# Performance work log

Hardware: AMD Instinct MI355X
Metric: run time of the kernel (lower is better)

The kernel has to match this reference:

```python
import jax, jax.numpy as jnp
import numpy as np

EMBED_DIM = 1024
NUM_HEADS = 16
HEAD_DIM = EMBED_DIM // NUM_HEADS
BOARD = 32
SEQ = BOARD * BOARD
BATCH = 16


def setup_inputs() -> dict:
    key = jax.random.key(0)
    ks = jax.random.split(key, 6)
    x = jax.random.normal(ks[0], (BATCH, SEQ, EMBED_DIM), dtype=jnp.float32)
    scale = 1.0 / np.sqrt(EMBED_DIM)
    Wq = jax.random.normal(ks[1], (EMBED_DIM, EMBED_DIM), dtype=jnp.float32) * scale
    Wk = jax.random.normal(ks[2], (EMBED_DIM, EMBED_DIM), dtype=jnp.float32) * scale
    Wv = jax.random.normal(ks[3], (EMBED_DIM, EMBED_DIM), dtype=jnp.float32) * scale
    Wo = jax.random.normal(ks[4], (EMBED_DIM, EMBED_DIM), dtype=jnp.float32) * scale
    rel_bias = jax.random.normal(ks[5], (NUM_HEADS, 2 * BOARD - 1), dtype=jnp.float32)
    return {"x": x, "Wq": Wq, "Wk": Wk, "Wv": Wv, "Wo": Wo, "rel_bias": rel_bias}


def _rel_indices():
    # coords of the flattened H*W grid
    idx = jnp.arange(SEQ)
    rows = idx // BOARD
    cols = idx % BOARD
    offset = BOARD - 1
    rel_x = cols[None, :] - cols[:, None] + offset  # [S, S]
    rel_y = rows[None, :] - rows[:, None] + offset  # [S, S]
    return rel_x, rel_y


def reference(x, Wq, Wk, Wv, Wo, rel_bias):
    B, S, E = x.shape
    H, D = NUM_HEADS, HEAD_DIM
    # projections (Linear with bias=False: x @ W.T; weights here stored as [E, E] applied as x @ W)
    q = (x @ Wq).reshape(B, S, H, D).transpose(0, 2, 1, 3)  # [B,H,S,D]
    k = (x @ Wk).reshape(B, S, H, D).transpose(0, 2, 1, 3)
    v = (x @ Wv).reshape(B, S, H, D).transpose(0, 2, 1, 3)
    scores = jnp.einsum('bhqd,bhkd->bhqk', q, k) / jnp.sqrt(jnp.float32(D))
    rel_x, rel_y = _rel_indices()
    bias = rel_bias[:, rel_x] + rel_bias[:, rel_y]  # [H, S, S]
    scores = scores + bias[None]
    attn = jax.nn.softmax(scores, axis=-1)
    out = jnp.einsum('bhqk,bhkd->bhqd', attn, v)
    out = out.transpose(0, 2, 1, 3).reshape(B, S, E)
    return out @ Wo
```

## Files before the change

kernel.cpp:

```cpp
#include <hip/hip_runtime.h>

#define SEQ   1024
#define EMBED 1024
#define NH    16
#define HD    64
#define NB    16

typedef float facc4 __attribute__((ext_vector_type(4)));
typedef float facc16 __attribute__((ext_vector_type(16)));
typedef short frag8 __attribute__((ext_vector_type(8)));
typedef short sv4 __attribute__((ext_vector_type(4)));

__device__ __forceinline__ unsigned short f2bf(float f) {
  union { float f; unsigned int u; } c; c.f = f;
  unsigned int u = c.u;
  u += 0x7FFFu + ((u >> 16) & 1u);
  return (unsigned short)(u >> 16);
}

__device__ __forceinline__ unsigned int pk_bf16(float lo, float hi) {
  unsigned int r;
  asm("v_cvt_pk_bf16_f32 %0, %1, %2" : "=v"(r) : "v"(lo), "v"(hi));
  return r;
}

__device__ __forceinline__ void gl_lds16(const void* g, void* l) {
  __builtin_amdgcn_global_load_lds(
      (const __attribute__((address_space(1))) unsigned int*)g,
      (__attribute__((address_space(3))) unsigned int*)l, 16, 0, 0);
}

__global__ __launch_bounds__(256) void convert_x_kernel(
    const float* __restrict__ x, unsigned short* __restrict__ xb, int n8) {
  int stride = gridDim.x * blockDim.x;
  for (int i = blockIdx.x * blockDim.x + threadIdx.x; i < n8; i += stride) {
    const float4* src = (const float4*)(x + (size_t)i * 8);
    float4 v0 = src[0], v1 = src[1];
    frag8 o;
    o[0] = f2bf(v0.x); o[1] = f2bf(v0.y); o[2] = f2bf(v0.z); o[3] = f2bf(v0.w);
    o[4] = f2bf(v1.x); o[5] = f2bf(v1.y); o[6] = f2bf(v1.z); o[7] = f2bf(v1.w);
    *(frag8*)(xb + (size_t)i * 8) = o;
  }
}

__global__ __launch_bounds__(256) void transpose_w_kernel(
    const float* W0, const float* W1, const float* W2, const float* W3,
    unsigned short* T0, unsigned short* T1, unsigned short* T2, unsigned short* T3) {
  __shared__ float tw[64][65];
  const float* W; unsigned short* T;
  switch (blockIdx.z) {
    case 0: W = W0; T = T0; break;
    case 1: W = W1; T = T1; break;
    case 2: W = W2; T = T2; break;
    default: W = W3; T = T3; break;
  }
  int k0 = blockIdx.y * 64, n0 = blockIdx.x * 64;
  int t = threadIdx.x;
#pragma unroll
  for (int rep = 0; rep < 4; ++rep) {
    int c = rep * 256 + t;
    int row = c >> 4, ch = c & 15;
    float4 v = *(const float4*)(W + (size_t)(k0 + row) * 1024 + n0 + ch * 4);
    tw[row][ch * 4 + 0] = v.x; tw[row][ch * 4 + 1] = v.y;
    tw[row][ch * 4 + 2] = v.z; tw[row][ch * 4 + 3] = v.w;
  }
  __syncthreads();
#pragma unroll
  for (int rep = 0; rep < 2; ++rep) {
    int c = rep * 256 + t;
    int nrow = c >> 3, ch = c & 7;
    frag8 o;
#pragma unroll
    for (int i = 0; i < 8; ++i) o[i] = (short)f2bf(tw[ch * 8 + i][nrow]);
    *(frag8*)(T + (size_t)(n0 + nrow) * 1024 + k0 + ch * 8) = o;
  }
}

template <int MODE>
__global__ __launch_bounds__(512, 2) void gemm256(
    const unsigned short* __restrict__ A, const unsigned short* __restrict__ Bt,
    unsigned short* __restrict__ qo, unsigned short* __restrict__ ko,
    unsigned short* __restrict__ vto, float* __restrict__ fo, int N) {
  __shared__ unsigned short a_s[2][256 * 64];
  __shared__ unsigned short b_s[2][256 * 64];
  const int tid = threadIdx.x;
  const int w = tid >> 6, l = tid & 63;
  const int l31 = l & 31, hi = l >> 5;
  const int wr = w >> 2, wc = w & 3;

  const int bid = blockIdx.x;
  const int xcd = bid & 7, j = bid >> 3;
  const int mt = xcd * 8 + (j & 7), nt = j >> 3;
  const int m0 = mt << 8, n0 = nt << 8;

  const int ldrow = l >> 3;
  const int swz8 = ((l & 7) ^ (ldrow & 7)) << 3;
  const unsigned short* Ab = A + (size_t)m0 * 1024;
  const unsigned short* Bb = Bt + (size_t)n0 * 1024;

  facc16 acc[4][2];
#pragma unroll
  for (int mi = 0; mi < 4; ++mi)
#pragma unroll
    for (int nj = 0; nj < 2; ++nj)
#pragma unroll
      for (int r = 0; r < 16; ++r) acc[mi][nj][r] = 0.f;

  auto STAGE = [&](int buf, int kt) {
#pragma unroll
    for (int i = 0; i < 4; ++i) {
      const int c = (w << 2) + i;
      gl_lds16(Ab + (size_t)kt * 64 + (size_t)((c << 3) + ldrow) * 1024 + swz8,
               &a_s[buf][c << 9]);
      gl_lds16(Bb + (size_t)kt * 64 + (size_t)((c << 3) + ldrow) * 1024 + swz8,
               &b_s[buf][c << 9]);
    }
  };

  STAGE(0, 0);
  STAGE(1, 1);
  asm volatile("s_waitcnt vmcnt(8)" ::: "memory");
  __builtin_amdgcn_s_barrier();
  __builtin_amdgcn_sched_barrier(0);

  const int rowA = (wr << 7) + l31;
  const int rowB = (wc << 6) + l31;
  const int swl = l31 & 7;

  for (int t = 0; t < 16; ++t) {
    const int cur = t & 1;
    const char* ap = (const char*)a_s[cur];
    const char* bp = (const char*)b_s[cur];
    frag8 af[4][2], bfv[2][2];

#pragma unroll
    for (int js2 = 0; js2 < 2; ++js2) {
      const int pc = (((js2 << 1) + hi) ^ swl) << 4;
#pragma unroll
      for (int mi = 0; mi < 4; ++mi)
        af[mi][js2] = *(const frag8*)(ap + (rowA + (mi << 5)) * 128 + pc);
#pragma unroll
      for (int nj = 0; nj < 2; ++nj)
        bfv[nj][js2] = *(const frag8*)(bp + (rowB + (nj << 5)) * 128 + pc);
    }
    __builtin_amdgcn_s_setprio(1);
#pragma unroll
    for (int js2 = 0; js2 < 2; ++js2)
#pragma unroll
      for (int mi = 0; mi < 4; ++mi)
#pragma unroll
        for (int nj = 0; nj < 2; ++nj)
          acc[mi][nj] = __builtin_amdgcn_mfma_f32_32x32x16_bf16(
              af[mi][js2], bfv[nj][js2], acc[mi][nj], 0, 0, 0);
    __builtin_amdgcn_s_setprio(0);

#pragma unroll
    for (int js2 = 0; js2 < 2; ++js2) {
      const int pc = ((((js2 + 2) << 1) + hi) ^ swl) << 4;
#pragma unroll
      for (int mi = 0; mi < 4; ++mi)
        af[mi][js2] = *(const frag8*)(ap + (rowA + (mi << 5)) * 128 + pc);
#pragma unroll
      for (int nj = 0; nj < 2; ++nj)
        bfv[nj][js2] = *(const frag8*)(bp + (rowB + (nj << 5)) * 128 + pc);
    }
    asm volatile("s_waitcnt lgkmcnt(0)" ::: "memory");
    __builtin_amdgcn_s_barrier();
    __builtin_amdgcn_sched_barrier(0);
    if (t + 2 < 16) STAGE(cur, t + 2);

    __builtin_amdgcn_s_setprio(1);
#pragma unroll
    for (int js2 = 0; js2 < 2; ++js2)
#pragma unroll
      for (int mi = 0; mi < 4; ++mi)
#pragma unroll
        for (int nj = 0; nj < 2; ++nj)
          acc[mi][nj] = __builtin_amdgcn_mfma_f32_32x32x16_bf16(
              af[mi][js2], bfv[nj][js2], acc[mi][nj], 0, 0, 0);
    __builtin_amdgcn_s_setprio(0);

    if (t < 14)       asm volatile("s_waitcnt vmcnt(8)" ::: "memory");
    else if (t == 14) asm volatile("s_waitcnt vmcnt(0)" ::: "memory");
    if (t < 15) {
      __builtin_amdgcn_s_barrier();
      __builtin_amdgcn_sched_barrier(0);
    }
  }

  const int m_base = m0 + (wr << 7);
  if (MODE == 0) {
    const int bb16 = (m_base >> 10) << 4;
#pragma unroll
    for (int nj = 0; nj < 2; ++nj) {
      const int n = n0 + (wc << 6) + (nj << 5) + l31;
      const int proj = n >> 10, rem = n & 1023;
      const int h = rem >> 6, d = rem & 63;
      const size_t bh16 = ((size_t)(bb16 + h)) << 16;
      if (proj == 2) {
#pragma unroll
        for (int mi = 0; mi < 4; ++mi)
#pragma unroll
          for (int rq = 0; rq < 4; ++rq) {
            const int s = (m_base + (mi << 5) + (rq << 3) + (hi << 2)) & 1023;
            sv4 pv;
#pragma unroll
            for (int rr = 0; rr < 4; ++rr)
              pv[rr] = (short)f2bf(acc[mi][nj][(rq << 2) + rr]);
            *(sv4*)(vto + bh16 + ((size_t)d << 10) + s) = pv;
          }
      } else {
        unsigned short* dst = (proj == 0) ? qo : ko;
#pragma unroll
        for (int mi = 0; mi < 4; ++mi)
#pragma unroll
          for (int r = 0; r < 16; ++r) {
            const int s = (m_base + (mi << 5) + (r & 3) + ((r >> 2) << 3) +
                           (hi << 2)) & 1023;
            dst[bh16 + (size_t)s * 64 + d] = f2bf(acc[mi][nj][r]);
          }
      }
    }
  } else {
#pragma unroll
    for (int nj = 0; nj < 2; ++nj) {
      const int n = n0 + (wc << 6) + (nj << 5) + l31;
#pragma unroll
      for (int mi = 0; mi < 4; ++mi)
#pragma unroll
        for (int r = 0; r < 16; ++r) {
          const int m = m_base + (mi << 5) + (r & 3) + ((r >> 2) << 3) + (hi << 2);
          fo[(size_t)m * N + n] = acc[mi][nj][r];
        }
    }
  }
}

__global__ __launch_bounds__(256) void attn_kernel(
    const unsigned short* __restrict__ q, const unsigned short* __restrict__ k,
    const unsigned short* __restrict__ vt, const float* __restrict__ rel_bias,
    unsigned short* __restrict__ ao) {
  __shared__ unsigned short k_s[64 * 64];
  __shared__ unsigned short v_s[64 * 64];
  __shared__ unsigned short o_s[4][32][72];
  __shared__ float rb_s[63];

  const int bid = blockIdx.x;
  const int xcd = bid & 7, jj = bid >> 3;
  const int bh = xcd * 32 + (jj >> 3), qt = jj & 7;
  const int b = bh >> 4, h = bh & 15;
  const int t = threadIdx.x, w = t >> 6, l = t & 63;
  const int l31 = l & 31, hi = l >> 5;

  if (t < 63) rb_s[t] = rel_bias[h * 63 + t] * 1.44269504f;

  const unsigned short* qg = q + (size_t)bh * (SEQ * 64);
  const unsigned short* kg = k + (size_t)bh * (SEQ * 64);
  const unsigned short* vg = vt + (size_t)bh * (64 * SEQ);

  const int q0 = qt * 128 + w * 32;
  const int qr = q0 >> 5;

  frag8 qf[4];
#pragma unroll
  for (int s = 0; s < 4; ++s)
    qf[s] = *(const frag8*)(qg + (size_t)(q0 + l31) * 64 + s * 16 + hi * 8);

  __syncthreads();

  float bx[16];
#pragma unroll
  for (int r = 0; r < 16; ++r) {
    const int kc = (r & 3) + 8 * (r >> 2) + 4 * hi;
    bx[r] = rb_s[kc - l31 + 31];
  }

  float m_run = -1e30f, lsum = 0.f;
  facc16 o0, o1;
#pragma unroll
  for (int i = 0; i < 16; ++i) { o0[i] = 0.f; o1[i] = 0.f; }

  const float C1 = 0.125f * 1.44269504f;

  for (int kt = 0; kt < 16; ++kt) {
    __syncthreads();
#pragma unroll
    for (int i = 0; i < 2; ++i) {
      const int c = i * 256 + t;
      const int row = c >> 3, ch = c & 7;
      const int sw = (ch ^ (row & 7)) << 3;
      const int base = (i * 256 + w * 64) << 3;
      gl_lds16(kg + (size_t)(kt * 64 + row) * 64 + sw, k_s + base);
      gl_lds16(vg + (size_t)row * SEQ + kt * 64 + sw, v_s + base);
    }
    __syncthreads();

    facc16 sa[2];
#pragma unroll
    for (int st = 0; st < 2; ++st) {
      facc16 z;
#pragma unroll
      for (int i = 0; i < 16; ++i) z[i] = 0.f;
#pragma unroll
      for (int s = 0; s < 4; ++s) {
        const int row = st * 32 + l31;
        const int byte_off = row * 128 + (((s * 2 + hi) ^ (row & 7)) << 4);
        frag8 kf = *(const frag8*)((const char*)k_s + byte_off);
        z = __builtin_amdgcn_mfma_f32_32x32x16_bf16(kf, qf[s], z, 0, 0, 0);
      }
      sa[st] = z;
    }

    const float by0 = rb_s[kt * 2 + 0 - qr + 31];
    const float by1 = rb_s[kt * 2 + 1 - qr + 31];
    float sc0[16], sc1[16];
#pragma unroll
    for (int r = 0; r < 16; ++r) {
      sc0[r] = __builtin_fmaf(sa[0][r], C1, bx[r]);
      sc1[r] = __builtin_fmaf(sa[1][r], C1, bx[r]);
    }
    float m0 = sc0[0], m1 = sc1[0];
#pragma unroll
    for (int r = 1; r < 16; ++r) { m0 = fmaxf(m0, sc0[r]); m1 = fmaxf(m1, sc1[r]); }
    float tm = fmaxf(m0 + by0, m1 + by1);
    tm = fmaxf(tm, __shfl_xor(tm, 32));
    if (!__all(tm <= m_run + 8.f)) {
      const float mn = fmaxf(m_run, tm);
      const float corr = __builtin_amdgcn_exp2f(m_run - mn);
      lsum *= corr;
#pragma unroll
      for (int i = 0; i < 16; ++i) { o0[i] *= corr; o1[i] *= corr; }
      m_run = mn;
    }
    const float mb0 = m_run - by0, mb1 = m_run - by1;
    float p0[16], p1[16];
    float ps = 0.f;
#pragma unroll
    for (int r = 0; r < 16; ++r) {
      p0[r] = __builtin_amdgcn_exp2f(sc0[r] - mb0);
      p1[r] = __builtin_amdgcn_exp2f(sc1[r] - mb1);
      ps += p0[r] + p1[r];
    }
    ps += __shfl_xor(ps, 32);
    lsum += ps;

    unsigned int fw[4][4];
#pragma unroll
    for (int ks = 0; ks < 4; ++ks) {
      const float* pp = (ks < 2) ? p0 : p1;
      const int R0 = (ks & 1) * 8;
      const int R1 = R0 + 4;
      const unsigned int w00 = pk_bf16(pp[R0 + 0], pp[R0 + 1]);
      const unsigned int w01 = pk_bf16(pp[R0 + 2], pp[R0 + 3]);
      const unsigned int w10 = pk_bf16(pp[R1 + 0], pp[R1 + 1]);
      const unsigned int w11 = pk_bf16(pp[R1 + 2], pp[R1 + 3]);
      const unsigned int s0 = hi ? w00 : w10;
      const unsigned int s1 = hi ? w01 : w11;
      const unsigned int r0 = __shfl_xor((int)s0, 32);
      const unsigned int r1 = __shfl_xor((int)s1, 32);
      fw[ks][0] = hi ? r0 : w00;
      fw[ks][1] = hi ? r1 : w01;
      fw[ks][2] = hi ? w10 : r0;
      fw[ks][3] = hi ? w11 : r1;
    }

#pragma unroll
    for (int ks = 0; ks < 4; ++ks) {
      frag8 pb;
      {
        union { unsigned int u[4]; frag8 f; } cv;
        cv.u[0] = fw[ks][0]; cv.u[1] = fw[ks][1];
        cv.u[2] = fw[ks][2]; cv.u[3] = fw[ks][3];
        pb = cv.f;
      }
      {
        const int row = l31;
        const int byte_off = row * 128 + (((ks * 2 + hi) ^ (row & 7)) << 4);
        frag8 vf = *(const frag8*)((const char*)v_s + byte_off);
        o0 = __builtin_amdgcn_mfma_f32_32x32x16_bf16(vf, pb, o0, 0, 0, 0);
      }
      {
        const int row = 32 + l31;
        const int byte_off = row * 128 + (((ks * 2 + hi) ^ (row & 7)) << 4);
        frag8 vf = *(const frag8*)((const char*)v_s + byte_off);
        o1 = __builtin_amdgcn_mfma_f32_32x32x16_bf16(vf, pb, o1, 0, 0, 0);
      }
    }
  }

  const float inv = __builtin_amdgcn_rcpf(lsum);
  unsigned short (*os)[72] = o_s[w];
#pragma unroll
  for (int dt = 0; dt < 2; ++dt) {
#pragma unroll
    for (int r = 0; r < 16; r += 2) {
      const int d = (r & 3) + 8 * (r >> 2) + 4 * hi + 32 * dt;
      const float e0 = (dt ? o1[r] : o0[r]) * inv;
      const float e1 = (dt ? o1[r + 1] : o0[r + 1]) * inv;
      *(unsigned int*)&os[l31][d] = pk_bf16(e0, e1);
    }
  }
#pragma unroll
  for (int i = 0; i < 4; ++i) {
    const int c = i * 64 + l;
    const int qrow = c >> 3, ch = c & 7;
    frag8 ov = *(const frag8*)(&os[qrow][ch * 8]);
    *(frag8*)(ao + ((size_t)(b * SEQ + q0 + qrow) * EMBED + h * 64 + ch * 8)) = ov;
  }
}

extern "C" void kernel_launch(void* const* d_in, const int* in_sizes, int n_in,
                              void* d_out, int out_size, void* d_ws, size_t ws_size,
                              hipStream_t stream) {
  (void)in_sizes; (void)n_in; (void)out_size; (void)ws_size;
  const float* x  = (const float*)d_in[0];
  const float* Wq = (const float*)d_in[1];
  const float* Wk = (const float*)d_in[2];
  const float* Wv = (const float*)d_in[3];
  const float* Wo = (const float*)d_in[4];
  const float* rb = (const float*)d_in[5];
  float* out = (float*)d_out;

  unsigned short* xb  = (unsigned short*)d_ws;
  unsigned short* wtq = xb + 16777216;
  unsigned short* wtk = wtq + 1048576;
  unsigned short* wtv = wtk + 1048576;
  unsigned short* wto = wtv + 1048576;
  unsigned short* qb  = wto + 1048576;
  unsigned short* kb  = qb + 16777216;
  unsigned short* aob = kb + 16777216;
  unsigned short* vtb = aob + 16777216;

  convert_x_kernel<<<4096, 256, 0, stream>>>(x, xb, 16777216 / 8);
  transpose_w_kernel<<<dim3(16, 16, 4), 256, 0, stream>>>(
      Wq, Wk, Wv, Wo, wtq, wtk, wtv, wto);
  gemm256<0><<<768, 512, 0, stream>>>(
      xb, wtq, qb, kb, vtb, nullptr, 3072);
  attn_kernel<<<2048, 256, 0, stream>>>(qb, kb, vtb, rb, aob);
  gemm256<1><<<256, 512, 0, stream>>>(
      aob, wto, nullptr, nullptr, nullptr, out, 1024);
}
```

Measured before the change: 289.0 us.

## Double-buffer K/V tiles in attention kernel with async prefetch and MFMA priority

Turns the single K/V LDS buffer into two buffers, so the next tile is fetched by global-to-LDS loads while the current tile is computed. Explicit vmcnt/lgkmcnt waits and raw barriers replace the __syncthreads pairs. It also raises wave priority around the MFMA sections, sets launch bounds to 4 blocks per CU, and lets the output staging buffer alias the K/V shared memory. The cost is more LDS per block and hand-placed waits that must exactly match the number of outstanding loads.

```diff
diff --git a/kernel.cpp b/kernel.cpp
--- a/kernel.cpp
+++ b/kernel.cpp
@@ -236,14 +236,14 @@
   }
 }
 
-__global__ __launch_bounds__(256) void attn_kernel(
+__global__ __launch_bounds__(256, 4) void attn_kernel(
     const unsigned short* __restrict__ q, const unsigned short* __restrict__ k,
     const unsigned short* __restrict__ vt, const float* __restrict__ rel_bias,
     unsigned short* __restrict__ ao) {
-  __shared__ unsigned short k_s[64 * 64];
-  __shared__ unsigned short v_s[64 * 64];
-  __shared__ unsigned short o_s[4][32][72];
+  __shared__ unsigned short smem[16384];
   __shared__ float rb_s[63];
+  unsigned short* k_s = smem;
+  unsigned short* v_s = smem + 8192;
 
   const int bid = blockIdx.x;
   const int xcd = bid & 7, jj = bid >> 3;
@@ -266,36 +266,53 @@
   for (int s = 0; s < 4; ++s)
     qf[s] = *(const frag8*)(qg + (size_t)(q0 + l31) * 64 + s * 16 + hi * 8);
 
-  __syncthreads();
-
-  float bx[16];
-#pragma unroll
-  for (int r = 0; r < 16; ++r) {
-    const int kc = (r & 3) + 8 * (r >> 2) + 4 * hi;
-    bx[r] = rb_s[kc - l31 + 31];
-  }
-
-  float m_run = -1e30f, lsum = 0.f;
-  facc16 o0, o1;
-#pragma unroll
-  for (int i = 0; i < 16; ++i) { o0[i] = 0.f; o1[i] = 0.f; }
-
-  const float C1 = 0.125f * 1.44269504f;
-
-  for (int kt = 0; kt < 16; ++kt) {
-    __syncthreads();
+  auto STAGE = [&](int buf, int kt) {
 #pragma unroll
     for (int i = 0; i < 2; ++i) {
       const int c = i * 256 + t;
       const int row = c >> 3, ch = c & 7;
       const int sw = (ch ^ (row & 7)) << 3;
-      const int base = (i * 256 + w * 64) << 3;
+      const int base = ((i * 256 + w * 64) << 3) + buf * 4096;
       gl_lds16(kg + (size_t)(kt * 64 + row) * 64 + sw, k_s + base);
       gl_lds16(vg + (size_t)row * SEQ + kt * 64 + sw, v_s + base);
     }
-    __syncthreads();
+  };
+  STAGE(0, 0);
+
+  asm volatile("s_waitcnt lgkmcnt(0)" ::: "memory");
+  __builtin_amdgcn_s_barrier();
+  __builtin_amdgcn_sched_barrier(0);
+
+  float bx[16];
+#pragma unroll
+  for (int r = 0; r < 16; ++r) {
+    const int kc = (r & 3) + 8 * (r >> 2) + 4 * hi;
+    bx[r] = rb_s[kc - l31 + 31];
+  }
+
+  float m_run = -1e30f, lsum = 0.f;
+  facc16 o0, o1;
+#pragma unroll
+  for (int i = 0; i < 16; ++i) { o0[i] = 0.f; o1[i] = 0.f; }
+
+  const float C1 = 0.125f * 1.44269504f;
+
+  for (int kt = 0; kt < 16; ++kt) {
+    const int p = kt & 1;
+    if (kt < 15) {
+      STAGE(p ^ 1, kt + 1);
+      asm volatile("s_waitcnt vmcnt(4)" ::: "memory");
+    } else {
+      asm volatile("s_waitcnt vmcnt(0)" ::: "memory");
+    }
+    __builtin_amdgcn_s_barrier();
+    __builtin_amdgcn_sched_barrier(0);
+
+    const char* kp = (const char*)(k_s + p * 4096);
+    const char* vp = (const char*)(v_s + p * 4096);
 
     facc16 sa[2];
+    __builtin_amdgcn_s_setprio(1);
 #pragma unroll
     for (int st = 0; st < 2; ++st) {
       facc16 z;
@@ -305,11 +322,12 @@
       for (int s = 0; s < 4; ++s) {
         const int row = st * 32 + l31;
         const int byte_off = row * 128 + (((s * 2 + hi) ^ (row & 7)) << 4);
-        frag8 kf = *(const frag8*)((const char*)k_s + byte_off);
+        frag8 kf = *(const frag8*)(kp + byte_off);
         z = __builtin_amdgcn_mfma_f32_32x32x16_bf16(kf, qf[s], z, 0, 0, 0);
       }
       sa[st] = z;
     }
+    __builtin_amdgcn_s_setprio(0);
 
     const float by0 = rb_s[kt * 2 + 0 - qr + 31];
     const float by1 = rb_s[kt * 2 + 1 - qr + 31];
@@ -364,6 +382,7 @@
       fw[ks][3] = hi ? w11 : r1;
     }
 
+    __builtin_amdgcn_s_setprio(1);
 #pragma unroll
     for (int ks = 0; ks < 4; ++ks) {
       frag8 pb;
@@ -376,20 +395,25 @@
       {
         const int row = l31;
         const int byte_off = row * 128 + (((ks * 2 + hi) ^ (row & 7)) << 4);
-        frag8 vf = *(const frag8*)((const char*)v_s + byte_off);
+        frag8 vf = *(const frag8*)(vp + byte_off);
         o0 = __builtin_amdgcn_mfma_f32_32x32x16_bf16(vf, pb, o0, 0, 0, 0);
       }
       {
         const int row = 32 + l31;
         const int byte_off = row * 128 + (((ks * 2 + hi) ^ (row & 7)) << 4);
-        frag8 vf = *(const frag8*)((const char*)v_s + byte_off);
+        frag8 vf = *(const frag8*)(vp + byte_off);
         o1 = __builtin_amdgcn_mfma_f32_32x32x16_bf16(vf, pb, o1, 0, 0, 0);
       }
     }
+    __builtin_amdgcn_s_setprio(0);
+
+    asm volatile("s_waitcnt lgkmcnt(0)" ::: "memory");
+    __builtin_amdgcn_s_barrier();
+    __builtin_amdgcn_sched_barrier(0);
   }
 
   const float inv = __builtin_amdgcn_rcpf(lsum);
-  unsigned short (*os)[72] = o_s[w];
+  unsigned short (*os)[72] = (unsigned short (*)[72])(smem + w * (32 * 72));
 #pragma unroll
   for (int dt = 0; dt < 2; ++dt) {
 #pragma unroll
@@ -400,6 +424,8 @@
       *(unsigned int*)&os[l31][d] = pk_bf16(e0, e1);
     }
   }
+  asm volatile("s_waitcnt lgkmcnt(0)" ::: "memory");
+  __builtin_amdgcn_sched_barrier(0);
 #pragma unroll
   for (int i = 0; i < 4; ++i) {
     const int c = i * 64 + l;
```

Measured after the change: 297.5 us. +3.0%, slower.
